# Kernel optimization log

Hardware: AMD Instinct MI355X
Metric: run time of the kernel (lower is better)

## Reference

```python
import jax, jax.numpy as jnp
import numpy as np

NF4 = jnp.array([-1.0, -0.6961928009986877, -0.5250730514526367, -0.39491748809814453,
                 -0.28444138169288635, -0.18477343022823334, -0.09105003625154495, 0.0,
                 0.07958029955625534, 0.16093020141124725, 0.24611230194568634,
                 0.33791524171829224, 0.44070982933044434, 0.5626170039176941,
                 0.7229568362236023, 1.0], dtype=jnp.float32)
BLOCK_SIZE = 64
SCALING = 32.0 / 16.0  # alpha / rank


def setup_inputs() -> dict:
    key = jax.random.key(0)
    k = jax.random.split(key, 6)
    B, S, IN, OUT, R = 4, 128, 4096, 11008, 16
    n_blocks = (OUT * IN) // BLOCK_SIZE  # 704512, exact (no padding needed)
    return {
        "x": jax.random.normal(k[0], (B, S, IN), jnp.float32),
        "weight_indices": jax.random.randint(k[1], (OUT, IN), 0, 16, dtype=jnp.int32),
        "weight_scales": jax.random.uniform(k[2], (n_blocks,), jnp.float32),
        "lora_A": jax.random.normal(k[3], (IN, R), jnp.float32),
        "lora_B": jax.random.normal(k[4], (R, OUT), jnp.float32),
        "bias": jax.random.normal(k[5], (OUT,), jnp.float32),
    }


def dequantize_nf4(indices, scales, shape):
    # LUT gather then blockwise absmax scale
    w = NF4[indices.reshape(-1)]                    # [out*in]
    w = w.reshape(-1, BLOCK_SIZE) * scales[:, None]  # [n_blocks, block]
    return w.reshape(shape)                          # [out, in]


def reference(x, weight_indices, weight_scales, lora_A, lora_B, bias):
    W = dequantize_nf4(weight_indices, weight_scales, weight_indices.shape)  # [out, in]
    base = jnp.einsum("bsi,oi->bso", x, W) + bias                            # F.linear
    lora = (x @ lora_A) @ lora_B                                             # low-rank path (dropout p=0 -> identity)
    return base + lora * SCALING
```

## Files before the change

### kernel.cpp

```cpp
#include <hip/hip_runtime.h>
#include <stdint.h>

typedef __bf16 bf16x8 __attribute__((ext_vector_type(8)));
typedef float f32x4 __attribute__((ext_vector_type(4)));
typedef unsigned short ushort_t;

#define N_OUT 11008
#define K_DIM 4096
#define M_DIM 512
#define BM 256
#define BN 64
#define BK 64
#define KHALF 2048
#define NT 32

__constant__ float c_nf4[16] = {
    -1.0f, -0.6961928009986877f, -0.5250730514526367f, -0.39491748809814453f,
    -0.28444138169288635f, -0.18477343022823334f, -0.09105003625154495f, 0.0f,
    0.07958029955625534f, 0.16093020141124725f, 0.24611230194568634f,
    0.33791524171829224f, 0.44070982933044434f, 0.5626170039176941f,
    0.7229568362236023f, 1.0f};

__device__ __forceinline__ uint32_t pkbf(float lo, float hi) {
  uint32_t ul = __builtin_bit_cast(uint32_t, lo);
  uint32_t uh = __builtin_bit_cast(uint32_t, hi);
  return ((ul + 0x8000u) >> 16) | ((uh + 0x8000u) & 0xffff0000u);
}

__device__ __forceinline__ void async16(const void* g, void* l) {
  __builtin_amdgcn_global_load_lds(
      (const __attribute__((address_space(1))) void*)g,
      (__attribute__((address_space(3))) void*)l, 16, 0, 0);
}

__device__ __forceinline__ bf16x8 ldfrag(const ushort_t* p) {
  uint4 r = *reinterpret_cast<const uint4*>(p);
  return __builtin_bit_cast(bf16x8, r);
}

__device__ __forceinline__ uint32_t dqb(uint32_t byte, float s, const float2* lut) {
  float2 l = lut[byte];
  return pkbf(l.x * s, l.y * s);
}

__global__ void k_prep(const float* __restrict__ x, const int* __restrict__ wi,
                       const float* __restrict__ lA, const float* __restrict__ lB,
                       ushort_t* __restrict__ xbf, ushort_t* __restrict__ xap,
                       ushort_t* __restrict__ btp, uint8_t* __restrict__ wpk) {
  const int b = blockIdx.x, t = threadIdx.x;
  if (b < 11008) {
    int g = b * 256 + t;
    int o = g >> 8;
    int kc = g & 255;
    const int4* src = (const int4*)(wi + (size_t)o * K_DIM + kc * 16);
    int4 a0 = src[0], a1 = src[1], a2 = src[2], a3 = src[3];
    uint32_t lo = (uint32_t)a0.x | ((uint32_t)a0.y << 4) | ((uint32_t)a0.z << 8) |
                  ((uint32_t)a0.w << 12) | ((uint32_t)a1.x << 16) |
                  ((uint32_t)a1.y << 20) | ((uint32_t)a1.z << 24) |
                  ((uint32_t)a1.w << 28);
    uint32_t hi = (uint32_t)a2.x | ((uint32_t)a2.y << 4) | ((uint32_t)a2.z << 8) |
                  ((uint32_t)a2.w << 12) | ((uint32_t)a3.x << 16) |
                  ((uint32_t)a3.y << 20) | ((uint32_t)a3.z << 24) |
                  ((uint32_t)a3.w << 28);
    ((uint2*)wpk)[g] = make_uint2(lo, hi);
  } else if (b < 12032) {
    int oc = (b - 11008) * 256 + t;
    int m = oc >> 9;
    int cr = oc & 511;
    int win = cr >> 3, cp = cr & 7;
    int c = cp ^ (m & 7);
    const float4* s4 = (const float4*)(x + (size_t)m * K_DIM + win * 64 + c * 8);
    float4 v0 = s4[0], v1 = s4[1];
    uint4 o;
    o.x = pkbf(v0.x, v0.y);
    o.y = pkbf(v0.z, v0.w);
    o.z = pkbf(v1.x, v1.y);
    o.w = pkbf(v1.z, v1.w);
    ((uint4*)xbf)[oc] = o;
  } else if (b < 12544) {
    __shared__ float red[256 * 17];
    int m = b - 12032;
    f32x4 ac0 = 0.f, ac1 = 0.f, ac2 = 0.f, ac3 = 0.f;
#pragma unroll
    for (int i = 0; i < 16; ++i) {
      int k = i * 256 + t;
      float xk = x[(size_t)m * K_DIM + k];
      const f32x4* l4 = (const f32x4*)(lA + (size_t)k * 16);
      ac0 += xk * l4[0];
      ac1 += xk * l4[1];
      ac2 += xk * l4[2];
      ac3 += xk * l4[3];
    }
#pragma unroll
    for (int r = 0; r < 4; ++r) {
      red[t * 17 + r] = ac0[r];
      red[t * 17 + 4 + r] = ac1[r];
      red[t * 17 + 8 + r] = ac2[r];
      red[t * 17 + 12 + r] = ac3[r];
    }
    __syncthreads();
#pragma unroll
    for (int s = 128; s >= 16; s >>= 1) {
      if (t < s)
        for (int r = 0; r < 16; ++r) red[t * 17 + r] += red[(t + s) * 17 + r];
      __syncthreads();
    }
    if (t < 32) {
      float v = 0.f;
      if (t < 16) {
        for (int p = 0; p < 16; ++p) v += red[p * 17 + t];
        v *= 2.0f;
      }
      uint32_t u = __builtin_bit_cast(uint32_t, v);
      xap[(size_t)m * 32 + t] = (ushort_t)((u + 0x8000u) >> 16);
    }
  } else {
    int o = (b - 12544) * 256 + t;
    uint32_t p[8];
#pragma unroll
    for (int j = 0; j < 8; ++j)
      p[j] = pkbf(lB[(size_t)(2 * j) * N_OUT + o], lB[(size_t)(2 * j + 1) * N_OUT + o]);
    uint4* dst = reinterpret_cast<uint4*>(btp + (size_t)o * 32);
    dst[0] = make_uint4(p[0], p[1], p[2], p[3]);
    dst[1] = make_uint4(p[4], p[5], p[6], p[7]);
    dst[2] = make_uint4(0u, 0u, 0u, 0u);
    dst[3] = make_uint4(0u, 0u, 0u, 0u);
  }
}

__launch_bounds__(256, 3)
__global__ void k_main(const ushort_t* __restrict__ xbf, const uint8_t* __restrict__ wpk,
                       const float* __restrict__ sc, const ushort_t* __restrict__ xap,
                       const ushort_t* __restrict__ btp,
                       const float* __restrict__ bias, float* __restrict__ out) {
  __shared__ __align__(16) ushort_t lds_a[BM * BK];
  __shared__ __align__(16) ushort_t lds_b[BN * 72];
  __shared__ float2 lutp[256];

  const int t = threadIdx.x;
  const int lane = t & 63;
  const int w = t >> 6;
  const int o0 = blockIdx.x * BN;
  const int m0 = blockIdx.y * BM;
  const int kh = blockIdx.z;
  const int k0 = kh * KHALF;

  lutp[t] = make_float2(c_nf4[t & 15], c_nf4[t >> 4]);

  const int brow = t >> 2, bq = t & 3;
  const uint2* gpb =
      (const uint2*)(wpk + (size_t)(o0 + brow) * (K_DIM / 2) + (k0 >> 1) + bq * 8);
  const float* gs = sc + (size_t)(o0 + brow) * 64 + kh * 32;
  ushort_t* lb = lds_b + brow * 72 + bq * 16;

  const ushort_t* ga =
      xbf + (size_t)(m0 + w * 64 + (lane >> 3)) * K_DIM + k0 + (lane & 7) * 8;
  ushort_t* la_dst = lds_a + w * 4096 + lane * 8;

  const int cl = lane & 15;
  f32x4 acc[4][4];
#pragma unroll
  for (int ni = 0; ni < 4; ++ni) {
    float b0 = (kh == 1) ? bias[o0 + ni * 16 + cl] : 0.f;
#pragma unroll
    for (int mi = 0; mi < 4; ++mi) acc[mi][ni] = (f32x4){b0, b0, b0, b0};
  }

  uint2 bp = gpb[0];
  float s = gs[0];
  uint4 braw;

  const ushort_t* afb = lds_a + (w * 64 + (lane & 15)) * BK;
  const int q = lane >> 4;
  const ushort_t* bfb = lds_b + (lane & 15) * 72 + q * 8;

#pragma unroll 1
  for (int kt = 0; kt < NT; ++kt) {
    __syncthreads();
    {
      uint32_t lo = bp.x, hi = bp.y;
      uint4 w0, w1;
      w0.x = dqb(lo & 255u, s, lutp);
      w0.y = dqb((lo >> 8) & 255u, s, lutp);
      w0.z = dqb((lo >> 16) & 255u, s, lutp);
      w0.w = dqb(lo >> 24, s, lutp);
      w1.x = dqb(hi & 255u, s, lutp);
      w1.y = dqb((hi >> 8) & 255u, s, lutp);
      w1.z = dqb((hi >> 16) & 255u, s, lutp);
      w1.w = dqb(hi >> 24, s, lutp);
      *reinterpret_cast<uint4*>(lb) = w0;
      *reinterpret_cast<uint4*>(lb + 8) = w1;
    }
#pragma unroll
    for (int j = 0; j < 8; ++j)
      async16(ga + (size_t)j * 8 * K_DIM + kt * BK, la_dst + j * 512);
    __syncthreads();
    if (kt + 1 < NT) {
      bp = gpb[(kt + 1) * 4];
      s = gs[kt + 1];
    } else if (kh == 1) {
      braw = *reinterpret_cast<const uint4*>(btp + (size_t)(o0 + brow) * 32 + bq * 8);
    }
#pragma unroll
    for (int kc = 0; kc < 2; ++kc) {
      const int cpr = ((kc * 4 + q) ^ (lane & 7)) * 8;
      bf16x8 av[4], bv[4];
#pragma unroll
      for (int mi = 0; mi < 4; ++mi) av[mi] = ldfrag(afb + mi * 16 * BK + cpr);
#pragma unroll
      for (int ni = 0; ni < 4; ++ni) bv[ni] = ldfrag(bfb + ni * 16 * 72 + kc * 32);
#pragma unroll
      for (int mi = 0; mi < 4; ++mi)
#pragma unroll
        for (int ni = 0; ni < 4; ++ni)
          acc[mi][ni] = __builtin_amdgcn_mfma_f32_16x16x32_bf16(av[mi], bv[ni],
                                                                acc[mi][ni], 0, 0, 0);
    }
  }

  if (kh == 1) {
    __syncthreads();
    *reinterpret_cast<uint4*>(lds_b + brow * 72 + bq * 8) = braw;
#pragma unroll
    for (int j = 0; j < 4; ++j)
      async16(xap + (size_t)(m0 + w * 64 + j * 16 + (lane >> 2)) * 32 + (lane & 3) * 8,
              lds_a + w * 2048 + j * 512 + lane * 8);
    __syncthreads();
    bf16x8 av[4], bv[4];
#pragma unroll
    for (int mi = 0; mi < 4; ++mi)
      av[mi] = ldfrag(lds_a + w * 2048 + (mi * 16 + (lane & 15)) * 32 + q * 8);
#pragma unroll
    for (int ni = 0; ni < 4; ++ni)
      bv[ni] = ldfrag(lds_b + (ni * 16 + (lane & 15)) * 72 + q * 8);
#pragma unroll
    for (int mi = 0; mi < 4; ++mi)
#pragma unroll
      for (int ni = 0; ni < 4; ++ni)
        acc[mi][ni] = __builtin_amdgcn_mfma_f32_16x16x32_bf16(av[mi], bv[ni],
                                                              acc[mi][ni], 0, 0, 0);
  }

  const int rg = q * 4;
#pragma unroll
  for (int ni = 0; ni < 4; ++ni) {
    int col = o0 + ni * 16 + cl;
#pragma unroll
    for (int mi = 0; mi < 4; ++mi) {
      int row0 = m0 + w * 64 + mi * 16 + rg;
      float* op = out + (size_t)row0 * N_OUT + col;
#pragma unroll
      for (int i = 0; i < 4; ++i) atomicAdd(op + (size_t)i * N_OUT, acc[mi][ni][i]);
    }
  }
}

extern "C" void kernel_launch(void* const* d_in, const int* in_sizes, int n_in,
                              void* d_out, int out_size, void* d_ws, size_t ws_size,
                              hipStream_t stream) {
  const float* x = (const float*)d_in[0];
  const int* wi = (const int*)d_in[1];
  const float* sc = (const float*)d_in[2];
  const float* lA = (const float*)d_in[3];
  const float* lB = (const float*)d_in[4];
  const float* bias = (const float*)d_in[5];
  float* out = (float*)d_out;

  char* wsb = (char*)d_ws;
  ushort_t* xbf = (ushort_t*)wsb;
  ushort_t* xap = (ushort_t*)(wsb + (4u << 20));
  ushort_t* btp = (ushort_t*)(wsb + (4u << 20) + (32u << 10));
  uint8_t* wpk = (uint8_t*)(wsb + (5u << 20));

  hipMemsetAsync(out, 0, (size_t)out_size, stream);
  k_prep<<<12587, 256, 0, stream>>>(x, wi, lA, lB, xbf, xap, btp, wpk);
  dim3 grid(N_OUT / BN, M_DIM / BM, 2);
  k_main<<<grid, 256, 0, stream>>>(xbf, wpk, sc, xap, btp, bias, out);
}
```

Baseline: 374.7 us.

## Double-buffer dequantized B tile to drop a barrier; coalesce NF4 packing loads

The dequantized weight tile in LDS now has two buffers that alternate by k-step. This lets the main loop drop the barrier at the top of each iteration and keep only one barrier per iteration. The A tile stays single-buffered, which relies on each wave reading only its own A rows. The prep kernel now packs each weight row with coalesced int4 loads and a shared-memory staging step, and the extra LDS per block may squeeze occupancy.

```diff
diff --git a/kernel.cpp b/kernel.cpp
--- a/kernel.cpp
+++ b/kernel.cpp
@@ -13,6 +13,7 @@
 #define BK 64
 #define KHALF 2048
 #define NT 32
+#define BSTRIDE (BN * 72)
 
 __constant__ float c_nf4[16] = {
     -1.0f, -0.6961928009986877f, -0.5250730514526367f, -0.39491748809814453f,
@@ -49,20 +50,17 @@
                        ushort_t* __restrict__ btp, uint8_t* __restrict__ wpk) {
   const int b = blockIdx.x, t = threadIdx.x;
   if (b < 11008) {
-    int g = b * 256 + t;
-    int o = g >> 8;
-    int kc = g & 255;
-    const int4* src = (const int4*)(wi + (size_t)o * K_DIM + kc * 16);
-    int4 a0 = src[0], a1 = src[1], a2 = src[2], a3 = src[3];
-    uint32_t lo = (uint32_t)a0.x | ((uint32_t)a0.y << 4) | ((uint32_t)a0.z << 8) |
-                  ((uint32_t)a0.w << 12) | ((uint32_t)a1.x << 16) |
-                  ((uint32_t)a1.y << 20) | ((uint32_t)a1.z << 24) |
-                  ((uint32_t)a1.w << 28);
-    uint32_t hi = (uint32_t)a2.x | ((uint32_t)a2.y << 4) | ((uint32_t)a2.z << 8) |
-                  ((uint32_t)a2.w << 12) | ((uint32_t)a3.x << 16) |
-                  ((uint32_t)a3.y << 20) | ((uint32_t)a3.z << 24) |
-                  ((uint32_t)a3.w << 28);
-    ((uint2*)wpk)[g] = make_uint2(lo, hi);
+    __shared__ uint16_t pk[1024];
+    const int4* src = (const int4*)(wi + (size_t)b * K_DIM);
+#pragma unroll
+    for (int j = 0; j < 4; ++j) {
+      int4 a = src[j * 256 + t];
+      pk[j * 256 + t] = (uint16_t)((uint32_t)a.x | ((uint32_t)a.y << 4) |
+                                   ((uint32_t)a.z << 8) | ((uint32_t)a.w << 12));
+    }
+    __syncthreads();
+    ((uint2*)(wpk + (size_t)b * (K_DIM / 2)))[t] =
+        *reinterpret_cast<const uint2*>(&pk[4 * t]);
   } else if (b < 12032) {
     int oc = (b - 11008) * 256 + t;
     int m = oc >> 9;
@@ -134,7 +132,7 @@
                        const ushort_t* __restrict__ btp,
                        const float* __restrict__ bias, float* __restrict__ out) {
   __shared__ __align__(16) ushort_t lds_a[BM * BK];
-  __shared__ __align__(16) ushort_t lds_b[BN * 72];
+  __shared__ __align__(16) ushort_t lds_b[2][BSTRIDE];
   __shared__ float2 lutp[256];
 
   const int t = threadIdx.x;
@@ -151,7 +149,7 @@
   const uint2* gpb =
       (const uint2*)(wpk + (size_t)(o0 + brow) * (K_DIM / 2) + (k0 >> 1) + bq * 8);
   const float* gs = sc + (size_t)(o0 + brow) * 64 + kh * 32;
-  ushort_t* lb = lds_b + brow * 72 + bq * 16;
+  ushort_t* lb = &lds_b[0][brow * 72 + bq * 16];
 
   const ushort_t* ga =
       xbf + (size_t)(m0 + w * 64 + (lane >> 3)) * K_DIM + k0 + (lane & 7) * 8;
@@ -172,11 +170,12 @@
 
   const ushort_t* afb = lds_a + (w * 64 + (lane & 15)) * BK;
   const int q = lane >> 4;
-  const ushort_t* bfb = lds_b + (lane & 15) * 72 + q * 8;
+  const ushort_t* bfb = &lds_b[0][(lane & 15) * 72 + q * 8];
+
+  __syncthreads();
 
 #pragma unroll 1
   for (int kt = 0; kt < NT; ++kt) {
-    __syncthreads();
     {
       uint32_t lo = bp.x, hi = bp.y;
       uint4 w0, w1;
@@ -188,8 +187,9 @@
       w1.y = dqb((hi >> 8) & 255u, s, lutp);
       w1.z = dqb((hi >> 16) & 255u, s, lutp);
       w1.w = dqb(hi >> 24, s, lutp);
-      *reinterpret_cast<uint4*>(lb) = w0;
-      *reinterpret_cast<uint4*>(lb + 8) = w1;
+      ushort_t* lbk = lb + (kt & 1) * BSTRIDE;
+      *reinterpret_cast<uint4*>(lbk) = w0;
+      *reinterpret_cast<uint4*>(lbk + 8) = w1;
     }
 #pragma unroll
     for (int j = 0; j < 8; ++j)
@@ -201,6 +201,7 @@
     } else if (kh == 1) {
       braw = *reinterpret_cast<const uint4*>(btp + (size_t)(o0 + brow) * 32 + bq * 8);
     }
+    const ushort_t* bfbk = bfb + (kt & 1) * BSTRIDE;
 #pragma unroll
     for (int kc = 0; kc < 2; ++kc) {
       const int cpr = ((kc * 4 + q) ^ (lane & 7)) * 8;
@@ -208,7 +209,7 @@
 #pragma unroll
       for (int mi = 0; mi < 4; ++mi) av[mi] = ldfrag(afb + mi * 16 * BK + cpr);
 #pragma unroll
-      for (int ni = 0; ni < 4; ++ni) bv[ni] = ldfrag(bfb + ni * 16 * 72 + kc * 32);
+      for (int ni = 0; ni < 4; ++ni) bv[ni] = ldfrag(bfbk + ni * 16 * 72 + kc * 32);
 #pragma unroll
       for (int mi = 0; mi < 4; ++mi)
 #pragma unroll
@@ -220,7 +221,7 @@
 
   if (kh == 1) {
     __syncthreads();
-    *reinterpret_cast<uint4*>(lds_b + brow * 72 + bq * 8) = braw;
+    *reinterpret_cast<uint4*>(&lds_b[0][brow * 72 + bq * 8]) = braw;
 #pragma unroll
     for (int j = 0; j < 4; ++j)
       async16(xap + (size_t)(m0 + w * 64 + j * 16 + (lane >> 2)) * 32 + (lane & 3) * 8,
@@ -232,7 +233,7 @@
       av[mi] = ldfrag(lds_a + w * 2048 + (mi * 16 + (lane & 15)) * 32 + q * 8);
 #pragma unroll
     for (int ni = 0; ni < 4; ++ni)
-      bv[ni] = ldfrag(lds_b + (ni * 16 + (lane & 15)) * 72 + q * 8);
+      bv[ni] = ldfrag(&lds_b[0][(ni * 16 + (lane & 15)) * 72 + q * 8]);
 #pragma unroll
     for (int mi = 0; mi < 4; ++mi)
 #pragma unroll
```

Result: no change. 372.6 us (-0.6%).
